# Kernel optimization log

Hardware: AMD Instinct MI355X
Metric: run time of the kernel (lower is better)

The kernel has to match this reference:

```python
import jax, jax.numpy as jnp
import numpy as np

DIM = 256
HEADS = 8
P = 8   # patch_size
S = 4   # stride


def _pos_index(p):
    # Swin-style relative position index, computed statically in numpy
    coord = np.arange(p)
    ii, jj = np.meshgrid(coord, coord, indexing='ij')
    cf = np.stack([ii.ravel(), jj.ravel()])              # [2, p*p]
    rel = cf[:, :, None] - cf[:, None, :]                # [2, P, P]
    rel = rel.transpose(1, 2, 0).copy()                  # [P, P, 2]
    rel[:, :, 0] += p - 1
    rel[:, :, 1] += p - 1
    rel[:, :, 0] *= 2 * p - 1
    return jnp.asarray(rel.sum(-1))                      # [P, P] int


def setup_inputs() -> dict:
    key = jax.random.key(0)
    k1, k2, k3, k4, k5 = jax.random.split(key, 5)
    x = jax.random.normal(k1, (2, DIM, 96, 96), jnp.float32)
    # depthwise 1x1 conv on 3*dim channels -> per-channel scale + bias
    qkv_w = jax.random.normal(k2, (3 * DIM,), jnp.float32) * 0.1 + 1.0
    qkv_b = jax.random.normal(k3, (3 * DIM,), jnp.float32) * 0.1
    # 1x1 conv dim->dim, no bias
    out_w = jax.random.normal(k4, (DIM, DIM), jnp.float32) * 0.05
    # relative position bias table, trunc_normal(std=0.02)
    pos_table = jax.random.normal(k5, ((2 * P - 1) ** 2, HEADS), jnp.float32) * 0.02
    return {"x": x, "qkv_w": qkv_w, "qkv_b": qkv_b, "out_w": out_w, "pos_table": pos_table}


def reference(x, qkv_w, qkv_b, out_w, pos_table):
    B, C, H, W = x.shape
    h, p, s = HEADS, P, S
    d = C // h
    pad = p - s
    # replicate pad right/bottom
    xp = jnp.pad(x, ((0, 0), (0, 0), (0, pad), (0, pad)), mode='edge')
    x3 = jnp.concatenate([xp, xp, xp], axis=1)           # [B, 3C, Hp, Wp]
    # depthwise 1x1 conv == per-channel affine
    qkv = x3 * qkv_w[None, :, None, None] + qkv_b[None, :, None, None]
    n = (H + pad - p) // s + 1                           # patches per side
    idx = (jnp.arange(n) * s)[:, None] + jnp.arange(p)[None, :]   # [n, p]
    # unfold: extract overlapping p x p patches with stride s
    t = qkv[:, :, idx, :]                                # [B, 3C, n, p, Wp]
    t = t[:, :, :, :, idx]                               # [B, 3C, n, p, n, p]
    t = t.transpose(0, 1, 2, 4, 3, 5)                    # [B, 3C, n, n, p, p]
    t = t.reshape(B, 3, h, d, n * n, p * p).transpose(1, 0, 2, 4, 5, 3)  # [3,B,h,N,P,d]
    q, k, v = t[0] * (d ** -0.5), t[1], t[2]
    bias = pos_table[_pos_index(p)]                      # [P, P, h]
    bias = bias.transpose(2, 0, 1)                       # [h, P, P]
    attn = jnp.einsum('bhnqd,bhnkd->bhnqk', q, k) + bias[None, :, None]
    attn = jax.nn.softmax(attn, axis=-1)
    out = jnp.einsum('bhnqk,bhnkd->bhnqd', attn, v)      # [B, h, N, P, d]
    # keep only the top-left stride x stride of each patch, then fold (non-overlap)
    out = out.reshape(B, h, n, n, p, p, d)[:, :, :, :, :s, :s]   # [B,h,n,n,s,s,d]
    out = out.transpose(0, 1, 6, 2, 4, 3, 5).reshape(B, C, H, W)
    return jnp.einsum('oc,bchw->bohw', out_w, out)
```

## Files before the change

### kernel.cpp

```cpp
#include <hip/hip_runtime.h>

typedef float f4 __attribute__((ext_vector_type(4)));
typedef float f32x4 __attribute__((ext_vector_type(4)));
typedef __bf16 bf16x8 __attribute__((ext_vector_type(8)));
typedef __bf16 bf16x4 __attribute__((ext_vector_type(4)));

#define NPSIDE 24

#define XS(ch_, r_, c_) xs[(ch_) * 253 + (r_) * 21 + (c_)]

__global__ __launch_bounds__(512, 2) void patch_attn(
    const float* __restrict__ x,
    const float* __restrict__ qkv_w,
    const float* __restrict__ qkv_b,
    const float* __restrict__ pos_table,
    const float* __restrict__ wmat,
    __bf16* __restrict__ mid,
    __bf16* __restrict__ wbf)
{
    __shared__ float xs[32 * 253];
    __shared__ __bf16 Ps[8][16][72];

    const int t = threadIdx.x;

    if (blockIdx.x < 32) {
        const int i = (blockIdx.x * 512 + t) * 4;
        const int o = i >> 8, c = i & 255;
        const f4 v = *(const f4*)&wmat[i];
        bf16x4 ov;
        #pragma unroll
        for (int j = 0; j < 4; ++j) ov[j] = (__bf16)v[j];
        *(bf16x4*)&wbf[((o >> 4) * 8 + (c >> 5)) * 512 + (o & 15) * 32 + (c & 31)] = ov;
    }

    int raw = blockIdx.x;
    const int sw = (raw & 7) * 144 + (raw >> 3);
    const int pgrp = sw % 72;
    const int bh   = sw / 72;
    const int head = bh & 7;
    const int b    = bh >> 3;
    const int ni0  = (pgrp / 6) * 2;
    const int nj0  = (pgrp % 6) * 4;
    const int c0   = head * 32;

    if (t < 384) {
        const int ch  = t / 12;
        const int row = t % 12;
        const int rg  = min(4 * ni0 + row, 95);
        const float* xrow = x + (((size_t)b * 256 + c0 + ch) * 96 + rg) * 96;
        float* xdst = &XS(ch, row, 0);
        const int cb = 4 * nj0;
        #pragma unroll
        for (int cg = 0; cg < 5; ++cg) {
            const int cg4 = cb + cg * 4;
            f4 v;
            if (cg4 <= 92) {
                v = *(const f4*)&xrow[cg4];
            } else {
                f4 u = *(const f4*)&xrow[92];
                v = (f4){u.w, u.w, u.w, u.w};
            }
            xdst[cg * 4 + 0] = v.x;
            xdst[cg * 4 + 1] = v.y;
            xdst[cg * 4 + 2] = v.z;
            xdst[cg * 4 + 3] = v.w;
        }
    }

    const int wv = t >> 6, l = t & 63;
    const int l16 = l & 15, lg = l >> 4;
    const float qscale = 0.17677669529663687f;

    float kw8[8], kb8[8], qw8[8], qb8[8];
    #pragma unroll
    for (int j = 0; j < 8; ++j) {
        const int c = c0 + 8 * lg + j;
        kw8[j] = qkv_w[256 + c];
        kb8[j] = qkv_b[256 + c];
        qw8[j] = qkv_w[c] * qscale;
        qb8[j] = qkv_b[c] * qscale;
    }
    float vw2[2], vb2[2];
    #pragma unroll
    for (int nt = 0; nt < 2; ++nt) {
        const int c = c0 + nt * 16 + l16;
        vw2[nt] = qkv_w[512 + c];
        vb2[nt] = qkv_b[512 + c];
    }

    __syncthreads();

    const int wni = wv >> 2, wnj = wv & 3;
    const int ni = ni0 + wni, nj = nj0 + wnj;
    const int rb = 4 * wni, cbl = 4 * wnj;

    bf16x8 qf;
    {
        const int qrow = rb + (l16 >> 2), qcol = cbl + (l16 & 3);
        #pragma unroll
        for (int j = 0; j < 8; ++j)
            qf[j] = (__bf16)(XS(8 * lg + j, qrow, qcol) * qw8[j] + qb8[j]);
    }

    const f32x4 zf = {0.f, 0.f, 0.f, 0.f};
    f32x4 sacc[4];
    #pragma unroll
    for (int t4 = 0; t4 < 4; ++t4) {
        const int px = l16 + 16 * t4;
        const int kr = rb + (px >> 3), kc = cbl + (px & 7);
        bf16x8 kf;
        #pragma unroll
        for (int j = 0; j < 8; ++j)
            kf[j] = (__bf16)(XS(8 * lg + j, kr, kc) * kw8[j] + kb8[j]);
        sacc[t4] = __builtin_amdgcn_mfma_f32_16x16x32_bf16(qf, kf, zf, 0, 0, 0);
    }

    float sv[4][4], rinv[4];
    #pragma unroll
    for (int r = 0; r < 4; ++r) {
        const int qrow = lg * 4 + r;
        const int qi = qrow >> 2, qj = qrow & 3;
        float m = -1e30f;
        #pragma unroll
        for (int t4 = 0; t4 < 4; ++t4) {
            const int kcol = l16 + 16 * t4;
            const int ki = kcol >> 3, kj = kcol & 7;
            const float s = sacc[t4][r]
                + pos_table[((qi - ki + 7) * 15 + (qj - kj + 7)) * 8 + head];
            sv[t4][r] = s;
            m = fmaxf(m, s);
        }
        #pragma unroll
        for (int off = 8; off >= 1; off >>= 1)
            m = fmaxf(m, __shfl_xor(m, off, 16));
        float sum = 0.f;
        #pragma unroll
        for (int t4 = 0; t4 < 4; ++t4) {
            const float p = __expf(sv[t4][r] - m);
            sv[t4][r] = p;
            sum += p;
        }
        #pragma unroll
        for (int off = 8; off >= 1; off >>= 1)
            sum += __shfl_xor(sum, off, 16);
        rinv[r] = 1.0f / sum;
        #pragma unroll
        for (int t4 = 0; t4 < 4; ++t4)
            Ps[wv][qrow][l16 + 16 * t4] = (__bf16)sv[t4][r];
    }

    f32x4 oa = zf, ob = zf;
    #pragma unroll
    for (int kt = 0; kt < 2; ++kt) {
        bf16x8 pf = *(const bf16x8*)&Ps[wv][l16][lg * 8 + 32 * kt];
        bf16x8 v0, v1;
        #pragma unroll
        for (int j = 0; j < 8; ++j) {
            const int px = kt * 32 + 8 * lg + j;
            const int vr = rb + (px >> 3), vc = cbl + (px & 7);
            v0[j] = (__bf16)(XS(l16,      vr, vc) * vw2[0] + vb2[0]);
            v1[j] = (__bf16)(XS(16 + l16, vr, vc) * vw2[1] + vb2[1]);
        }
        oa = __builtin_amdgcn_mfma_f32_16x16x32_bf16(pf, v0, oa, 0, 0, 0);
        ob = __builtin_amdgcn_mfma_f32_16x16x32_bf16(pf, v1, ob, 0, 0, 0);
    }

    const int pbase = ni * 384 + lg * 96 + nj * 4;
    __bf16* mbb = mid + (size_t)b * 9216 * 256;
    #pragma unroll
    for (int r = 0; r < 4; ++r) {
        const int p = pbase + r;
        __bf16* dst = mbb + ((p >> 4) * 8 + head) * 512 + (p & 15) * 32;
        dst[l16]      = (__bf16)(oa[r] * rinv[r]);
        dst[16 + l16] = (__bf16)(ob[r] * rinv[r]);
    }
}

__global__ __launch_bounds__(64) void proj(
    const __bf16* __restrict__ wbf,
    const __bf16* __restrict__ mid,
    float* __restrict__ y)
{
    const int l = threadIdx.x;
    const int l16 = l & 15, lg = l >> 4;
    const int fragoff = l16 * 32 + lg * 8;

    int raw = blockIdx.x;
    const int tid = (raw & 7) * 288 + (raw >> 3);
    const int b   = tid / 1152;
    const int r2  = tid % 1152;
    const int pt  = r2 >> 1;
    const int ot0 = (r2 & 1) * 8;

    const __bf16* midb = mid + ((size_t)b * 9216 + (size_t)pt * 16) * 256;

    bf16x8 bfr[8];
    #pragma unroll
    for (int kt = 0; kt < 8; ++kt)
        bfr[kt] = *(const bf16x8*)&midb[kt * 512 + fragoff];

    const int p = pt * 16 + l16;
    #pragma unroll
    for (int ot = 0; ot < 8; ++ot) {
        f32x4 acc = {0.f, 0.f, 0.f, 0.f};
        #pragma unroll
        for (int kt = 0; kt < 8; ++kt) {
            const bf16x8 af =
                *(const bf16x8*)&wbf[((ot0 + ot) * 8 + kt) * 512 + fragoff];
            acc = __builtin_amdgcn_mfma_f32_16x16x32_bf16(af, bfr[kt], acc, 0, 0, 0);
        }
        const int o = (ot0 + ot) * 16 + lg * 4;
        float* yb = y + ((size_t)b * 256 + o) * 9216 + p;
        #pragma unroll
        for (int r = 0; r < 4; ++r)
            yb[(size_t)r * 9216] = acc[r];
    }
}

extern "C" void kernel_launch(void* const* d_in, const int* in_sizes, int n_in,
                              void* d_out, int out_size, void* d_ws, size_t ws_size,
                              hipStream_t stream) {
    const float* x         = (const float*)d_in[0];
    const float* qkv_w     = (const float*)d_in[1];
    const float* qkv_b     = (const float*)d_in[2];
    const float* out_w     = (const float*)d_in[3];
    const float* pos_table = (const float*)d_in[4];
    float* y    = (float*)d_out;
    __bf16* mid = (__bf16*)d_ws;
    __bf16* wbf = (__bf16*)((char*)d_ws + (12u << 20));

    patch_attn<<<dim3(1152), dim3(512), 0, stream>>>(
        x, qkv_w, qkv_b, pos_table, out_w, mid, wbf);
    proj<<<dim3(2304), dim3(64), 0, stream>>>(
        wbf, mid, y);
}
```

Measured before the change: 40.10 us.

## Stage projection weights in LDS and share across four waves per block

The projection kernel now uses 256-thread blocks. Each block copies a 64-output slice of the bf16 weight matrix into shared memory once, and its four waves each process a different 16-pixel tile against it. This cuts redundant global/L2 weight fetches per wave. In exchange, each activation tile is now loaded by four blocks instead of two, and a block-wide sync plus 32 KB of LDS are added.

```diff
diff --git a/kernel.cpp b/kernel.cpp
--- a/kernel.cpp
+++ b/kernel.cpp
@@ -176,44 +176,64 @@
     }
 }
 
-__global__ __launch_bounds__(64) void proj(
+__global__ __launch_bounds__(256) void proj(
     const __bf16* __restrict__ wbf,
     const __bf16* __restrict__ mid,
     float* __restrict__ y)
 {
-    const int l = threadIdx.x;
+    __shared__ __align__(16) __bf16 wlds[4][8][512];
+
+    const int t  = threadIdx.x;
+    const int wv = t >> 6;
+    const int l  = t & 63;
     const int l16 = l & 15, lg = l >> 4;
     const int fragoff = l16 * 32 + lg * 8;
 
-    int raw = blockIdx.x;
-    const int tid = (raw & 7) * 288 + (raw >> 3);
-    const int b   = tid / 1152;
-    const int r2  = tid % 1152;
-    const int pt  = r2 >> 1;
-    const int ot0 = (r2 & 1) * 8;
+    const int raw = blockIdx.x;
+    const int xcd = raw & 7;
+    const int seq = raw >> 3;
+    const int chunk = xcd * 18 + (seq >> 3);
+    const int rem   = seq & 7;
+    const int b     = rem >> 2;
+    const int og4   = rem & 3;
+    const int ot0   = og4 * 4;
+    const int pt    = chunk * 4 + wv;
+
+    {
+        const bf16x8* wsrc = (const bf16x8*)&wbf[(size_t)ot0 * 8 * 512];
+        bf16x8* wdst = (bf16x8*)&wlds[0][0][0];
+        #pragma unroll
+        for (int i = 0; i < 8; ++i)
+            wdst[t + 256 * i] = wsrc[t + 256 * i];
+    }
+    __syncthreads();
 
     const __bf16* midb = mid + ((size_t)b * 9216 + (size_t)pt * 16) * 256;
-
     bf16x8 bfr[8];
     #pragma unroll
     for (int kt = 0; kt < 8; ++kt)
         bfr[kt] = *(const bf16x8*)&midb[kt * 512 + fragoff];
 
+    f32x4 acc[4];
+    #pragma unroll
+    for (int ot = 0; ot < 4; ++ot) acc[ot] = (f32x4){0.f, 0.f, 0.f, 0.f};
+
+    #pragma unroll
+    for (int ot = 0; ot < 4; ++ot)
+        #pragma unroll
+        for (int kt = 0; kt < 8; ++kt) {
+            const bf16x8 af = *(const bf16x8*)&wlds[ot][kt][fragoff];
+            acc[ot] = __builtin_amdgcn_mfma_f32_16x16x32_bf16(af, bfr[kt], acc[ot], 0, 0, 0);
+        }
+
     const int p = pt * 16 + l16;
     #pragma unroll
-    for (int ot = 0; ot < 8; ++ot) {
-        f32x4 acc = {0.f, 0.f, 0.f, 0.f};
-        #pragma unroll
-        for (int kt = 0; kt < 8; ++kt) {
-            const bf16x8 af =
-                *(const bf16x8*)&wbf[((ot0 + ot) * 8 + kt) * 512 + fragoff];
-            acc = __builtin_amdgcn_mfma_f32_16x16x32_bf16(af, bfr[kt], acc, 0, 0, 0);
-        }
+    for (int ot = 0; ot < 4; ++ot) {
         const int o = (ot0 + ot) * 16 + lg * 4;
         float* yb = y + ((size_t)b * 256 + o) * 9216 + p;
         #pragma unroll
         for (int r = 0; r < 4; ++r)
-            yb[(size_t)r * 9216] = acc[r];
+            yb[(size_t)r * 9216] = acc[ot][r];
     }
 }
 
@@ -231,6 +251,6 @@
 
     patch_attn<<<dim3(1152), dim3(512), 0, stream>>>(
         x, qkv_w, qkv_b, pos_table, out_w, mid, wbf);
-    proj<<<dim3(2304), dim3(64), 0, stream>>>(
+    proj<<<dim3(1152), dim3(256), 0, stream>>>(
         wbf, mid, y);
 }
```

After: 35.96 us. -10.3%, faster.
